# Optimization experiments

Measured on AMD Instinct MI355X. Metric: run time of the kernel, lower is better.

Reference implementation:

```python
import jax, jax.numpy as jnp
import numpy as np

N_ANCHORS = 10647
N_CLASSES = 80
N_OUT = 5 + N_CLASSES
N_GT = 2048
POS_IOU = 0.7
NEG_IOU = 0.3
N_SAMPLE = 256
POS_RATIO = 0.5


def _cxcy_to_corners(b):
    return jnp.concatenate([b[:, :2] - b[:, 2:4] / 2, b[:, :2] + b[:, 2:4] / 2], axis=-1)


def _iou(a, b):
    # a: [N,4] corner boxes, b: [M,4] corner boxes -> [N,M]
    lt = jnp.maximum(a[:, None, :2], b[None, :, :2])
    rb = jnp.minimum(a[:, None, 2:], b[None, :, 2:])
    wh = jnp.clip(rb - lt, 0.0)
    inter = wh[..., 0] * wh[..., 1]
    area_a = (a[:, 2] - a[:, 0]) * (a[:, 3] - a[:, 1])
    area_b = (b[:, 2] - b[:, 0]) * (b[:, 3] - b[:, 1])
    return inter / (area_a[:, None] + area_b[None, :] - inter)


def _bce_logits(x, t):
    # numerically stable BCEWithLogits, elementwise
    return jnp.maximum(x, 0.0) - x * t + jnp.log1p(jnp.exp(-jnp.abs(x)))


def _demote_first(labels, value, excess):
    # demote the first `excess` anchors (in index order) whose label == value to -1,
    # mirroring torch's nonzero()[randperm(excess)] which always hits the first
    # `excess` entries of the nonzero list
    m = labels == value
    cum = jnp.cumsum(m.astype(jnp.int32))
    return jnp.where(m & (cum <= excess), -1.0, labels)


def _generate_targets(priors, gt_boxes, gt_labels):
    ious = _iou(_cxcy_to_corners(priors[:, :4]), _cxcy_to_corners(gt_boxes))  # [N, M]
    gt_max_index = jnp.argmax(ious, axis=0)       # [M] best anchor per gt
    anchor_max_ious = jnp.max(ious, axis=1)       # [N]
    anchor_max_index = jnp.argmax(ious, axis=1)   # [N]
    labels = jnp.full((N_ANCHORS,), -1.0, dtype=ious.dtype)
    labels = labels.at[gt_max_index].set(1.0)
    labels = jnp.where(anchor_max_ious >= POS_IOU, 1.0, labels)
    labels = jnp.where(anchor_max_ious < NEG_IOU, 0.0, labels)
    n_pos_quota = int(POS_RATIO * N_SAMPLE)
    n_pos_actual = jnp.sum(labels == 1.0)
    labels = _demote_first(labels, 1.0, jnp.maximum(n_pos_actual - n_pos_quota, 0))
    n_neg_req = N_SAMPLE - jnp.sum(labels == 1.0)
    n_neg_actual = jnp.sum(labels == 0.0)
    labels = _demote_first(labels, 0.0, jnp.maximum(n_neg_actual - n_neg_req, 0))
    anchor_gt_box = gt_boxes[anchor_max_index]    # [N,4] matched gt box per anchor
    anchor_cls = gt_labels[anchor_max_index] + 5  # [N] one-hot class column per anchor
    targets = jnp.zeros((N_ANCHORS, N_OUT), dtype=gt_boxes.dtype)
    targets = targets.at[:, :4].set(anchor_gt_box)
    targets = targets.at[:, 4].set(labels)
    targets = targets.at[jnp.arange(N_ANCHORS), anchor_cls].set(1.0)
    return targets


def _forward(predictions, gt_boxes, gt_labels, priors):
    targets = _generate_targets(priors, gt_boxes, gt_labels)
    pred = predictions[0]                          # [N, N_OUT]
    labels = targets[:, 4]
    pos = (labels == 1.0).astype(pred.dtype)
    neg = (labels == 0.0).astype(pred.dtype)
    n_pos = jnp.maximum(jnp.sum(pos), 1.0)
    n_neg = jnp.maximum(jnp.sum(neg), 1.0)
    # masked-mean MSE over x,y,w,h on positive anchors
    diff2 = (pred[:, :4] - targets[:, :4]) ** 2
    loss_box = jnp.sum(pos[:, None] * diff2, axis=0) / n_pos
    loss_conf_obj = jnp.sum(pos * _bce_logits(pred[:, 4], targets[:, 4])) / n_pos
    loss_conf_nonobj = jnp.sum(neg * _bce_logits(pred[:, 4], targets[:, 4])) / n_neg
    loss_class = jnp.sum(pos[:, None] * _bce_logits(pred[:, 5:], targets[:, 5:])) / (n_pos * N_CLASSES)
    total_loss = jnp.sum(loss_box) + loss_conf_obj + loss_conf_nonobj + loss_class
    return pred, total_loss


def setup_inputs() -> dict:
    key = jax.random.key(0)
    k1, k2, k3, k4 = jax.random.split(key, 4)
    predictions = jax.random.normal(k1, (1, N_ANCHORS, N_OUT), dtype=jnp.float32)
    gt_boxes = jax.random.uniform(k2, (N_GT, 4), dtype=jnp.float32, minval=0.05, maxval=0.95)
    gt_labels = jax.random.randint(k3, (N_GT,), 0, N_CLASSES)
    priors = jax.random.uniform(k4, (N_ANCHORS, N_OUT), dtype=jnp.float32, minval=0.05, maxval=0.95)
    return {"predictions": predictions, "gt_boxes": gt_boxes, "gt_labels": gt_labels, "priors": priors}


def reference(predictions, gt_boxes, gt_labels, priors):
    return _forward(predictions, gt_boxes, gt_labels, priors)
```

## Files before the change

### kernel.cpp

```cpp
#include <hip/hip_runtime.h>
#include <math.h>

#define N_ANCH 10647
#define N_GT   2048
#define N_OUTC 85
#define PRED_ELEMS (N_ANCH * N_OUTC)
#define PRED_V4    (PRED_ELEMS / 4)
#define GT_CHUNK   128
#define A_CHUNK    128

struct WS {
    unsigned long long akey[N_ANCH];
    unsigned long long gkey[N_GT];
    unsigned int flags[N_ANCH];
    int poslist[128];
    int neglist[256];
    int counts[2];
    float part_a[128];
    float part_cls[128];
    float part_neg[2];
};

__device__ __forceinline__ float bce(float x, float t) {
    return fmaxf(x, 0.0f) - x * t + log1pf(expf(-fabsf(x)));
}

__global__ __launch_bounds__(256) void k_prep(const float* __restrict__ pred,
                                              float* __restrict__ out,
                                              WS* __restrict__ ws) {
    int idx = blockIdx.x * 256 + threadIdx.x;
    if (idx < PRED_V4)
        ((float4*)out)[idx] = ((const float4*)pred)[idx];
    if (idx == 0) {
        out[PRED_ELEMS - 3] = pred[PRED_ELEMS - 3];
        out[PRED_ELEMS - 2] = pred[PRED_ELEMS - 2];
        out[PRED_ELEMS - 1] = pred[PRED_ELEMS - 1];
    }
    if (idx < N_ANCH) { ws->akey[idx] = 0ull; ws->flags[idx] = 0u; }
    if (idx < N_GT)   { ws->gkey[idx] = 0ull; }
}

__global__ __launch_bounds__(256) void k_amax(const float* __restrict__ priors,
                                              const float* __restrict__ gtb,
                                              WS* __restrict__ ws) {
    __shared__ float4 sb[GT_CHUNK];
    __shared__ float  sba[GT_CHUNK];
    int tx = threadIdx.x;
    int jbase = blockIdx.y * GT_CHUNK;
    if (tx < GT_CHUNK) {
        int j = jbase + tx;
        float cx = gtb[j*4+0], cy = gtb[j*4+1], w = gtb[j*4+2], h = gtb[j*4+3];
        float4 c = make_float4(cx - w*0.5f, cy - h*0.5f, cx + w*0.5f, cy + h*0.5f);
        sb[tx] = c;
        sba[tx] = (c.z - c.x) * (c.w - c.y);
    }
    __syncthreads();
    int i = blockIdx.x * 256 + tx;
    float4 a = make_float4(0.f, 0.f, 0.f, 0.f);
    float aa = 0.f;
    if (i < N_ANCH) {
        float cx = priors[i*N_OUTC+0], cy = priors[i*N_OUTC+1];
        float w  = priors[i*N_OUTC+2], h  = priors[i*N_OUTC+3];
        a = make_float4(cx - w*0.5f, cy - h*0.5f, cx + w*0.5f, cy + h*0.5f);
        aa = (a.z - a.x) * (a.w - a.y);
    }
    unsigned long long best = 0ull;
#pragma unroll 4
    for (int jj = 0; jj < GT_CHUNK; ++jj) {
        float4 b = sb[jj]; float ab = sba[jj];
        float lx = fmaxf(a.x, b.x), ly = fmaxf(a.y, b.y);
        float rx = fminf(a.z, b.z), ry = fminf(a.w, b.w);
        float ww = fmaxf(rx - lx, 0.0f), hh = fmaxf(ry - ly, 0.0f);
        float inter = ww * hh;
        float uni = (aa + ab) - inter;
        float iou = inter / uni;
        unsigned long long key =
            ((unsigned long long)__float_as_uint(iou) << 32) |
            (unsigned)(~(unsigned)(jbase + jj));
        best = (key > best) ? key : best;
    }
    if (i < N_ANCH) atomicMax(&ws->akey[i], best);
}

__global__ __launch_bounds__(256) void k_gmax(const float* __restrict__ priors,
                                              const float* __restrict__ gtb,
                                              WS* __restrict__ ws) {
    __shared__ float4 sa[A_CHUNK];
    __shared__ float  saa[A_CHUNK];
    int tx = threadIdx.x;
    int ibase = blockIdx.y * A_CHUNK;
    if (tx < A_CHUNK) {
        int i = ibase + tx;
        float4 c = make_float4(0.f, 0.f, 0.f, 0.f);
        float ar = 0.f;
        if (i < N_ANCH) {
            float cx = priors[i*N_OUTC+0], cy = priors[i*N_OUTC+1];
            float w  = priors[i*N_OUTC+2], h  = priors[i*N_OUTC+3];
            c = make_float4(cx - w*0.5f, cy - h*0.5f, cx + w*0.5f, cy + h*0.5f);
            ar = (c.z - c.x) * (c.w - c.y);
        }
        sa[tx] = c; saa[tx] = ar;
    }
    __syncthreads();
    int j = blockIdx.x * 256 + tx;
    float cx = gtb[j*4+0], cy = gtb[j*4+1], w = gtb[j*4+2], h = gtb[j*4+3];
    float4 b = make_float4(cx - w*0.5f, cy - h*0.5f, cx + w*0.5f, cy + h*0.5f);
    float ab = (b.z - b.x) * (b.w - b.y);
    unsigned long long best = 0ull;
#pragma unroll 4
    for (int ii = 0; ii < A_CHUNK; ++ii) {
        float4 a = sa[ii]; float aa = saa[ii];
        float lx = fmaxf(a.x, b.x), ly = fmaxf(a.y, b.y);
        float rx = fminf(a.z, b.z), ry = fminf(a.w, b.w);
        float ww = fmaxf(rx - lx, 0.0f), hh = fmaxf(ry - ly, 0.0f);
        float inter = ww * hh;
        float uni = (aa + ab) - inter;
        float iou = inter / uni;
        unsigned long long key =
            ((unsigned long long)__float_as_uint(iou) << 32) |
            (unsigned)(~(unsigned)(ibase + ii));
        best = (key > best) ? key : best;
    }
    atomicMax(&ws->gkey[j], best);
}

__global__ __launch_bounds__(1024) void k_labels(WS* __restrict__ ws) {
    __shared__ int w1[16], w2[16];
    int tid = threadIdx.x, lane = tid & 63, wid = tid >> 6;

    for (int j = tid; j < N_GT; j += 1024) {
        unsigned ai = ~(unsigned)(ws->gkey[j]);
        ws->flags[ai] = 1u;
    }
    __syncthreads();

    const int NCH = (N_ANCH + 1023) / 1024;
    int cp = 0, cn = 0;
    for (int c = 0; c < NCH; ++c) {
        int i = c * 1024 + tid;
        if (i < N_ANCH) {
            float amax = __uint_as_float((unsigned)(ws->akey[i] >> 32));
            int lab = (amax < 0.3f) ? 0 : ((amax >= 0.7f || ws->flags[i]) ? 1 : -1);
            cp += (lab == 1); cn += (lab == 0);
        }
    }
    for (int o = 32; o; o >>= 1) { cp += __shfl_down(cp, o); cn += __shfl_down(cn, o); }
    if (lane == 0) { w1[wid] = cp; w2[wid] = cn; }
    __syncthreads();
    int npa = 0, nna = 0;
    for (int w = 0; w < 16; ++w) { npa += w1[w]; nna += w2[w]; }
    __syncthreads();

    int excess_pos = (npa > 128) ? (npa - 128) : 0;
    int n_pos_f = npa - excess_pos;
    int n_neg_req = 256 - n_pos_f;
    int excess_neg = (nna > n_neg_req) ? (nna - n_neg_req) : 0;
    int n_neg_f = nna - excess_neg;

    int run_p = 0, run_n = 0;
    for (int c = 0; c < NCH; ++c) {
        int i = c * 1024 + tid;
        int lab = -2;
        if (i < N_ANCH) {
            float amax = __uint_as_float((unsigned)(ws->akey[i] >> 32));
            lab = (amax < 0.3f) ? 0 : ((amax >= 0.7f || ws->flags[i]) ? 1 : -1);
        }
        bool f1 = (lab == 1), f0 = (lab == 0);
        unsigned long long b1 = __ballot(f1), b0 = __ballot(f0);
        unsigned long long pm = (2ull << lane) - 1ull;
        int r1 = __popcll(b1 & pm), r0 = __popcll(b0 & pm);
        if (lane == 0) { w1[wid] = __popcll(b1); w2[wid] = __popcll(b0); }
        __syncthreads();
        int p1 = 0, t1 = 0, p0 = 0, t0 = 0;
        for (int w = 0; w < 16; ++w) {
            int v1 = w1[w], v0 = w2[w];
            t1 += v1; t0 += v0;
            if (w < wid) { p1 += v1; p0 += v0; }
        }
        if (f1) {
            int cum = run_p + p1 + r1;
            if (cum > excess_pos) ws->poslist[cum - excess_pos - 1] = i;
        }
        if (f0) {
            int cum = run_n + p0 + r0;
            if (cum > excess_neg) ws->neglist[cum - excess_neg - 1] = i;
        }
        run_p += t1; run_n += t0;
        __syncthreads();
    }
    if (tid == 0) { ws->counts[0] = n_pos_f; ws->counts[1] = n_neg_f; }
}

__global__ __launch_bounds__(128) void k_loss(const float* __restrict__ pred,
                                              const float* __restrict__ gtb,
                                              const int* __restrict__ gtl,
                                              WS* __restrict__ ws) {
    __shared__ float r[4];
    int b = blockIdx.x, t = threadIdx.x, lane = t & 63, wid = t >> 6;
    if (b < 128) {
        int npf = ws->counts[0];
        float at = 0.f, ct = 0.f;
        if (b < npf && t < N_OUTC) {
            int i = ws->poslist[b];
            unsigned am = ~(unsigned)(ws->akey[i]);
            float p = pred[i * N_OUTC + t];
            if (t < 4) {
                float d = p - gtb[am * 4 + t];
                at = d * d;
            } else if (t == 4) {
                at = bce(p, 1.0f);
            } else {
                int cls = gtl[am] + 5;
                ct = bce(p, (t == cls) ? 1.0f : 0.0f);
            }
        }
        for (int o = 32; o; o >>= 1) { at += __shfl_down(at, o); ct += __shfl_down(ct, o); }
        if (lane == 0) { r[wid] = at; r[2 + wid] = ct; }
        __syncthreads();
        if (t == 0) { ws->part_a[b] = r[0] + r[1]; ws->part_cls[b] = r[2] + r[3]; }
    } else {
        int nnf = ws->counts[1];
        int idx = (b - 128) * 128 + t;
        float v = 0.f;
        if (idx < nnf) {
            int i = ws->neglist[idx];
            v = bce(pred[i * N_OUTC + 4], 0.0f);
        }
        for (int o = 32; o; o >>= 1) v += __shfl_down(v, o);
        if (lane == 0) r[wid] = v;
        __syncthreads();
        if (t == 0) ws->part_neg[b - 128] = r[0] + r[1];
    }
}

__global__ __launch_bounds__(128) void k_final(WS* __restrict__ ws, float* __restrict__ out) {
    __shared__ float r[4];
    int t = threadIdx.x, lane = t & 63, wid = t >> 6;
    float A = ws->part_a[t], C = ws->part_cls[t];
    for (int o = 32; o; o >>= 1) { A += __shfl_down(A, o); C += __shfl_down(C, o); }
    if (lane == 0) { r[wid] = A; r[2 + wid] = C; }
    __syncthreads();
    if (t == 0) {
        float As = r[0] + r[1], Cs = r[2] + r[3];
        float CN = ws->part_neg[0] + ws->part_neg[1];
        float np = fmaxf((float)ws->counts[0], 1.0f);
        float nn = fmaxf((float)ws->counts[1], 1.0f);
        out[PRED_ELEMS] = As / np + CN / nn + Cs / (np * 80.0f);
    }
}

extern "C" void kernel_launch(void* const* d_in, const int* in_sizes, int n_in,
                              void* d_out, int out_size, void* d_ws, size_t ws_size,
                              hipStream_t stream) {
    const float* pred   = (const float*)d_in[0];
    const float* gtb    = (const float*)d_in[1];
    const int*   gtl    = (const int*)d_in[2];
    const float* priors = (const float*)d_in[3];
    float* out = (float*)d_out;
    WS* ws = (WS*)d_ws;

    k_prep<<<dim3((PRED_V4 + 255) / 256), 256, 0, stream>>>(pred, out, ws);
    k_amax<<<dim3((N_ANCH + 255) / 256, N_GT / GT_CHUNK), 256, 0, stream>>>(priors, gtb, ws);
    k_gmax<<<dim3(N_GT / 256, (N_ANCH + A_CHUNK - 1) / A_CHUNK), 256, 0, stream>>>(priors, gtb, ws);
    k_labels<<<1, 1024, 0, stream>>>(ws);
    k_loss<<<130, 128, 0, stream>>>(pred, gtb, gtl, ws);
    k_final<<<1, 128, 0, stream>>>(ws, out);
}
```

Baseline: 78.66 us.

## Merge IoU passes into one launch and fold loss into label kernel

Box corners and areas are now computed once in the prep kernel and stored in the workspace. The per-anchor and per-GT argmax passes are merged into a single kernel launch that splits its blocks between the two roles. The inner loop tracks a float max and an index instead of a 64-bit key compare. The loss and final reduction are folded into the single-block label kernel using shared-memory lists, which cuts the launch count from six to three. In exchange, the loss work now runs serially in one block instead of spreading across 130 blocks.

```diff
diff --git a/kernel.cpp b/kernel.cpp
--- a/kernel.cpp
+++ b/kernel.cpp
@@ -6,19 +6,15 @@
 #define N_OUTC 85
 #define PRED_ELEMS (N_ANCH * N_OUTC)
 #define PRED_V4    (PRED_ELEMS / 4)
-#define GT_CHUNK   128
-#define A_CHUNK    128
 
 struct WS {
     unsigned long long akey[N_ANCH];
     unsigned long long gkey[N_GT];
     unsigned int flags[N_ANCH];
-    int poslist[128];
-    int neglist[256];
-    int counts[2];
-    float part_a[128];
-    float part_cls[128];
-    float part_neg[2];
+    float4 ac[N_ANCH];
+    float  aa[N_ANCH];
+    float4 gc[N_GT];
+    float  ga[N_GT];
 };
 
 __device__ __forceinline__ float bce(float x, float t) {
@@ -26,6 +22,8 @@
 }
 
 __global__ __launch_bounds__(256) void k_prep(const float* __restrict__ pred,
+                                              const float* __restrict__ gtb,
+                                              const float* __restrict__ priors,
                                               float* __restrict__ out,
                                               WS* __restrict__ ws) {
     int idx = blockIdx.x * 256 + threadIdx.x;
@@ -36,96 +34,100 @@
         out[PRED_ELEMS - 2] = pred[PRED_ELEMS - 2];
         out[PRED_ELEMS - 1] = pred[PRED_ELEMS - 1];
     }
-    if (idx < N_ANCH) { ws->akey[idx] = 0ull; ws->flags[idx] = 0u; }
-    if (idx < N_GT)   { ws->gkey[idx] = 0ull; }
-}
-
-__global__ __launch_bounds__(256) void k_amax(const float* __restrict__ priors,
-                                              const float* __restrict__ gtb,
-                                              WS* __restrict__ ws) {
-    __shared__ float4 sb[GT_CHUNK];
-    __shared__ float  sba[GT_CHUNK];
-    int tx = threadIdx.x;
-    int jbase = blockIdx.y * GT_CHUNK;
-    if (tx < GT_CHUNK) {
-        int j = jbase + tx;
-        float cx = gtb[j*4+0], cy = gtb[j*4+1], w = gtb[j*4+2], h = gtb[j*4+3];
+    if (idx < N_ANCH) {
+        ws->akey[idx] = 0ull;
+        ws->flags[idx] = 0u;
+        float cx = priors[idx*N_OUTC+0], cy = priors[idx*N_OUTC+1];
+        float w  = priors[idx*N_OUTC+2], h  = priors[idx*N_OUTC+3];
         float4 c = make_float4(cx - w*0.5f, cy - h*0.5f, cx + w*0.5f, cy + h*0.5f);
-        sb[tx] = c;
-        sba[tx] = (c.z - c.x) * (c.w - c.y);
-    }
-    __syncthreads();
-    int i = blockIdx.x * 256 + tx;
-    float4 a = make_float4(0.f, 0.f, 0.f, 0.f);
-    float aa = 0.f;
-    if (i < N_ANCH) {
-        float cx = priors[i*N_OUTC+0], cy = priors[i*N_OUTC+1];
-        float w  = priors[i*N_OUTC+2], h  = priors[i*N_OUTC+3];
-        a = make_float4(cx - w*0.5f, cy - h*0.5f, cx + w*0.5f, cy + h*0.5f);
-        aa = (a.z - a.x) * (a.w - a.y);
-    }
-    unsigned long long best = 0ull;
+        ws->ac[idx] = c;
+        ws->aa[idx] = (c.z - c.x) * (c.w - c.y);
+    }
+    if (idx < N_GT) {
+        ws->gkey[idx] = 0ull;
+        float cx = gtb[idx*4+0], cy = gtb[idx*4+1], w = gtb[idx*4+2], h = gtb[idx*4+3];
+        float4 c = make_float4(cx - w*0.5f, cy - h*0.5f, cx + w*0.5f, cy + h*0.5f);
+        ws->gc[idx] = c;
+        ws->ga[idx] = (c.z - c.x) * (c.w - c.y);
+    }
+}
+
+__global__ __launch_bounds__(256) void k_iou(WS* __restrict__ ws) {
+    __shared__ float4 sc[128];
+    __shared__ float  sa[128];
+    int b = blockIdx.x, tx = threadIdx.x;
+    if (b < 672) {
+        int bx = b % 42, by = b / 42;
+        int jbase = by * 128;
+        if (tx < 128) { sc[tx] = ws->gc[jbase + tx]; sa[tx] = ws->ga[jbase + tx]; }
+        __syncthreads();
+        int i = bx * 256 + tx;
+        bool valid = (i < N_ANCH);
+        float4 a = make_float4(0.f, 0.f, 0.f, 0.f);
+        float aa_ = 0.f;
+        if (valid) { a = ws->ac[i]; aa_ = ws->aa[i]; }
+        float bi = -1.0f; int bj = 0;
 #pragma unroll 4
-    for (int jj = 0; jj < GT_CHUNK; ++jj) {
-        float4 b = sb[jj]; float ab = sba[jj];
-        float lx = fmaxf(a.x, b.x), ly = fmaxf(a.y, b.y);
-        float rx = fminf(a.z, b.z), ry = fminf(a.w, b.w);
-        float ww = fmaxf(rx - lx, 0.0f), hh = fmaxf(ry - ly, 0.0f);
-        float inter = ww * hh;
-        float uni = (aa + ab) - inter;
-        float iou = inter / uni;
+        for (int jj = 0; jj < 128; ++jj) {
+            float4 g = sc[jj]; float ga_ = sa[jj];
+            float lx = fmaxf(a.x, g.x), ly = fmaxf(a.y, g.y);
+            float rx = fminf(a.z, g.z), ry = fminf(a.w, g.w);
+            float w  = fmaxf(rx - lx, 0.0f), h = fmaxf(ry - ly, 0.0f);
+            float inter = w * h;
+            float iou = inter / ((aa_ + ga_) - inter);
+            bool gt = iou > bi;
+            bi = gt ? iou : bi;
+            bj = gt ? jj : bj;
+        }
+        if (valid) {
+            unsigned long long key =
+                ((unsigned long long)__float_as_uint(bi) << 32) |
+                (unsigned)(~(unsigned)(jbase + bj));
+            atomicMax(&ws->akey[i], key);
+        }
+    } else {
+        int b2 = b - 672;
+        int bx = b2 % 8, by = b2 / 8;
+        int ibase = by * 128;
+        if (tx < 128) {
+            int i = ibase + tx;
+            if (i < N_ANCH) { sc[tx] = ws->ac[i]; sa[tx] = ws->aa[i]; }
+            else { sc[tx] = make_float4(0.f, 0.f, 0.f, 0.f); sa[tx] = 0.f; }
+        }
+        __syncthreads();
+        int j = bx * 256 + tx;
+        float4 g = ws->gc[j]; float ga_ = ws->ga[j];
+        float bi = -1.0f; int bii = 0;
+#pragma unroll 4
+        for (int ii = 0; ii < 128; ++ii) {
+            float4 a = sc[ii]; float aa_ = sa[ii];
+            float lx = fmaxf(a.x, g.x), ly = fmaxf(a.y, g.y);
+            float rx = fminf(a.z, g.z), ry = fminf(a.w, g.w);
+            float w  = fmaxf(rx - lx, 0.0f), h = fmaxf(ry - ly, 0.0f);
+            float inter = w * h;
+            float iou = inter / ((aa_ + ga_) - inter);
+            bool gt = iou > bi;
+            bi = gt ? iou : bi;
+            bii = gt ? ii : bii;
+        }
         unsigned long long key =
-            ((unsigned long long)__float_as_uint(iou) << 32) |
-            (unsigned)(~(unsigned)(jbase + jj));
-        best = (key > best) ? key : best;
-    }
-    if (i < N_ANCH) atomicMax(&ws->akey[i], best);
-}
-
-__global__ __launch_bounds__(256) void k_gmax(const float* __restrict__ priors,
-                                              const float* __restrict__ gtb,
-                                              WS* __restrict__ ws) {
-    __shared__ float4 sa[A_CHUNK];
-    __shared__ float  saa[A_CHUNK];
-    int tx = threadIdx.x;
-    int ibase = blockIdx.y * A_CHUNK;
-    if (tx < A_CHUNK) {
-        int i = ibase + tx;
-        float4 c = make_float4(0.f, 0.f, 0.f, 0.f);
-        float ar = 0.f;
-        if (i < N_ANCH) {
-            float cx = priors[i*N_OUTC+0], cy = priors[i*N_OUTC+1];
-            float w  = priors[i*N_OUTC+2], h  = priors[i*N_OUTC+3];
-            c = make_float4(cx - w*0.5f, cy - h*0.5f, cx + w*0.5f, cy + h*0.5f);
-            ar = (c.z - c.x) * (c.w - c.y);
-        }
-        sa[tx] = c; saa[tx] = ar;
-    }
-    __syncthreads();
-    int j = blockIdx.x * 256 + tx;
-    float cx = gtb[j*4+0], cy = gtb[j*4+1], w = gtb[j*4+2], h = gtb[j*4+3];
-    float4 b = make_float4(cx - w*0.5f, cy - h*0.5f, cx + w*0.5f, cy + h*0.5f);
-    float ab = (b.z - b.x) * (b.w - b.y);
-    unsigned long long best = 0ull;
-#pragma unroll 4
-    for (int ii = 0; ii < A_CHUNK; ++ii) {
-        float4 a = sa[ii]; float aa = saa[ii];
-        float lx = fmaxf(a.x, b.x), ly = fmaxf(a.y, b.y);
-        float rx = fminf(a.z, b.z), ry = fminf(a.w, b.w);
-        float ww = fmaxf(rx - lx, 0.0f), hh = fmaxf(ry - ly, 0.0f);
-        float inter = ww * hh;
-        float uni = (aa + ab) - inter;
-        float iou = inter / uni;
-        unsigned long long key =
-            ((unsigned long long)__float_as_uint(iou) << 32) |
-            (unsigned)(~(unsigned)(ibase + ii));
-        best = (key > best) ? key : best;
-    }
-    atomicMax(&ws->gkey[j], best);
-}
-
-__global__ __launch_bounds__(1024) void k_labels(WS* __restrict__ ws) {
+            ((unsigned long long)__float_as_uint(bi) << 32) |
+            (unsigned)(~(unsigned)(ibase + bii));
+        atomicMax(&ws->gkey[j], key);
+    }
+}
+
+__global__ __launch_bounds__(1024) void k_tail(const float* __restrict__ pred,
+                                               const float* __restrict__ gtb,
+                                               const int* __restrict__ gtl,
+                                               WS* __restrict__ ws,
+                                               float* __restrict__ out) {
     __shared__ int w1[16], w2[16];
+    __shared__ float fr[48];
+    __shared__ int poslist[128];
+    __shared__ int poscls[128];
+    __shared__ float posbox[128][4];
+    __shared__ int neglist[256];
     int tid = threadIdx.x, lane = tid & 63, wid = tid >> 6;
 
     for (int j = tid; j < N_GT; j += 1024) {
@@ -179,73 +181,56 @@
         }
         if (f1) {
             int cum = run_p + p1 + r1;
-            if (cum > excess_pos) ws->poslist[cum - excess_pos - 1] = i;
+            if (cum > excess_pos) {
+                int slot = cum - excess_pos - 1;
+                poslist[slot] = i;
+                unsigned am = ~(unsigned)(ws->akey[i]);
+                poscls[slot] = gtl[am] + 5;
+                posbox[slot][0] = gtb[am*4+0];
+                posbox[slot][1] = gtb[am*4+1];
+                posbox[slot][2] = gtb[am*4+2];
+                posbox[slot][3] = gtb[am*4+3];
+            }
         }
         if (f0) {
             int cum = run_n + p0 + r0;
-            if (cum > excess_neg) ws->neglist[cum - excess_neg - 1] = i;
+            if (cum > excess_neg) neglist[cum - excess_neg - 1] = i;
         }
         run_p += t1; run_n += t0;
         __syncthreads();
     }
-    if (tid == 0) { ws->counts[0] = n_pos_f; ws->counts[1] = n_neg_f; }
-}
-
-__global__ __launch_bounds__(128) void k_loss(const float* __restrict__ pred,
-                                              const float* __restrict__ gtb,
-                                              const int* __restrict__ gtl,
-                                              WS* __restrict__ ws) {
-    __shared__ float r[4];
-    int b = blockIdx.x, t = threadIdx.x, lane = t & 63, wid = t >> 6;
-    if (b < 128) {
-        int npf = ws->counts[0];
-        float at = 0.f, ct = 0.f;
-        if (b < npf && t < N_OUTC) {
-            int i = ws->poslist[b];
-            unsigned am = ~(unsigned)(ws->akey[i]);
-            float p = pred[i * N_OUTC + t];
-            if (t < 4) {
-                float d = p - gtb[am * 4 + t];
-                at = d * d;
-            } else if (t == 4) {
-                at = bce(p, 1.0f);
-            } else {
-                int cls = gtl[am] + 5;
-                ct = bce(p, (t == cls) ? 1.0f : 0.0f);
-            }
-        }
-        for (int o = 32; o; o >>= 1) { at += __shfl_down(at, o); ct += __shfl_down(ct, o); }
-        if (lane == 0) { r[wid] = at; r[2 + wid] = ct; }
-        __syncthreads();
-        if (t == 0) { ws->part_a[b] = r[0] + r[1]; ws->part_cls[b] = r[2] + r[3]; }
-    } else {
-        int nnf = ws->counts[1];
-        int idx = (b - 128) * 128 + t;
-        float v = 0.f;
-        if (idx < nnf) {
-            int i = ws->neglist[idx];
-            v = bce(pred[i * N_OUTC + 4], 0.0f);
-        }
-        for (int o = 32; o; o >>= 1) v += __shfl_down(v, o);
-        if (lane == 0) r[wid] = v;
-        __syncthreads();
-        if (t == 0) ws->part_neg[b - 128] = r[0] + r[1];
-    }
-}
-
-__global__ __launch_bounds__(128) void k_final(WS* __restrict__ ws, float* __restrict__ out) {
-    __shared__ float r[4];
-    int t = threadIdx.x, lane = t & 63, wid = t >> 6;
-    float A = ws->part_a[t], C = ws->part_cls[t];
-    for (int o = 32; o; o >>= 1) { A += __shfl_down(A, o); C += __shfl_down(C, o); }
-    if (lane == 0) { r[wid] = A; r[2 + wid] = C; }
-    __syncthreads();
-    if (t == 0) {
-        float As = r[0] + r[1], Cs = r[2] + r[3];
-        float CN = ws->part_neg[0] + ws->part_neg[1];
-        float np = fmaxf((float)ws->counts[0], 1.0f);
-        float nn = fmaxf((float)ws->counts[1], 1.0f);
-        out[PRED_ELEMS] = As / np + CN / nn + Cs / (np * 80.0f);
+
+    float acc_a = 0.f, acc_c = 0.f, acc_n = 0.f;
+    int nterms = n_pos_f * N_OUTC;
+    for (int t = tid; t < nterms; t += 1024) {
+        int pi = t / N_OUTC, col = t - pi * N_OUTC;
+        int i = poslist[pi];
+        float p = pred[i * N_OUTC + col];
+        if (col < 4) {
+            float d = p - posbox[pi][col];
+            acc_a += d * d;
+        } else if (col == 4) {
+            acc_a += bce(p, 1.0f);
+        } else {
+            acc_c += bce(p, (col == poscls[pi]) ? 1.0f : 0.0f);
+        }
+    }
+    for (int t = tid; t < n_neg_f; t += 1024) {
+        acc_n += bce(pred[neglist[t] * N_OUTC + 4], 0.0f);
+    }
+    for (int o = 32; o; o >>= 1) {
+        acc_a += __shfl_down(acc_a, o);
+        acc_c += __shfl_down(acc_c, o);
+        acc_n += __shfl_down(acc_n, o);
+    }
+    if (lane == 0) { fr[wid] = acc_a; fr[16 + wid] = acc_c; fr[32 + wid] = acc_n; }
+    __syncthreads();
+    if (tid == 0) {
+        float A = 0.f, C = 0.f, Nn = 0.f;
+        for (int w = 0; w < 16; ++w) { A += fr[w]; C += fr[16 + w]; Nn += fr[32 + w]; }
+        float np = fmaxf((float)n_pos_f, 1.0f);
+        float nn = fmaxf((float)n_neg_f, 1.0f);
+        out[PRED_ELEMS] = A / np + Nn / nn + C / (np * 80.0f);
     }
 }
 
@@ -259,10 +244,7 @@
     float* out = (float*)d_out;
     WS* ws = (WS*)d_ws;
 
-    k_prep<<<dim3((PRED_V4 + 255) / 256), 256, 0, stream>>>(pred, out, ws);
-    k_amax<<<dim3((N_ANCH + 255) / 256, N_GT / GT_CHUNK), 256, 0, stream>>>(priors, gtb, ws);
-    k_gmax<<<dim3(N_GT / 256, (N_ANCH + A_CHUNK - 1) / A_CHUNK), 256, 0, stream>>>(priors, gtb, ws);
-    k_labels<<<1, 1024, 0, stream>>>(ws);
-    k_loss<<<130, 128, 0, stream>>>(pred, gtb, gtl, ws);
-    k_final<<<1, 128, 0, stream>>>(ws, out);
-}
+    k_prep<<<dim3((PRED_V4 + 255) / 256), 256, 0, stream>>>(pred, gtb, priors, out, ws);
+    k_iou<<<dim3(672 + 672), 256, 0, stream>>>(ws);
+    k_tail<<<1, 1024, 0, stream>>>(pred, gtb, gtl, ws, out);
+}
```

Measured after the change: 85.64 us. +8.9%, slower.
